# Kernel tuning notes

Hardware: AMD Instinct MI355X
Metric: run time of the kernel (lower is better)

## Reference

```python
import jax, jax.numpy as jnp
import numpy as np

N0, N1, N2 = 331776, 36864, 4096   # src nodes block0, mid nodes, final items
E0, E1, EP = 294912, 32768, 4096   # edges block0, block1, pos/neg edges
F_RAW, D, H = 128, 256, 512        # raw feat dim, hidden_dims_sum, 2*hidden
N_NODES = 1000000                  # global graph node count (scorer bias)


def setup_inputs() -> dict:
    key = jax.random.key(0)
    ks = jax.random.split(key, 24)
    ri = lambda k, n, hi: jax.random.randint(k, (n,), 0, hi, dtype=jnp.int64 if False else jnp.int32).astype(jnp.int32)
    s = 0.05
    return {
        "feat0": jax.random.normal(ks[0], (N0, F_RAW), jnp.float32),
        "feat_dst": jax.random.normal(ks[1], (N2, F_RAW), jnp.float32),
        "weights0": jax.random.uniform(ks[2], (E0,), jnp.float32),
        "weights1": jax.random.uniform(ks[3], (E1,), jnp.float32),
        "W_proj": jax.random.normal(ks[4], (F_RAW, D), jnp.float32) * s,
        "b_proj": jnp.zeros((D,), jnp.float32),
        "Q1": jax.random.normal(ks[5], (D, H), jnp.float32) * s,
        "bq1": jnp.zeros((H,), jnp.float32),
        "W1": jax.random.normal(ks[6], (D + H, D), jnp.float32) * s,
        "bw1": jnp.zeros((D,), jnp.float32),
        "Q2": jax.random.normal(ks[7], (D, H), jnp.float32) * s,
        "bq2": jnp.zeros((H,), jnp.float32),
        "W2": jax.random.normal(ks[8], (D + H, D), jnp.float32) * s,
        "bw2": jnp.zeros((D,), jnp.float32),
        "bias": jnp.zeros((N_NODES,), jnp.float32),
        "block0_src": ri(ks[9], E0, N0),
        "block0_dst": ri(ks[10], E0, N1),
        "block1_src": ri(ks[11], E1, N1),
        "block1_dst": ri(ks[12], E1, N2),
        "pos_src": ri(ks[13], EP, N2),
        "pos_dst": ri(ks[14], EP, N2),
        "neg_src": ri(ks[15], EP, N2),
        "neg_dst": ri(ks[16], EP, N2),
        "nid": ri(ks[17], N2, N_NODES),
    }


def _l2norm(z):
    n = jnp.linalg.norm(z, axis=1, keepdims=True)
    return z / jnp.where(n == 0, 1.0, n)


def _sage_conv(h_src, h_dst, src, dst, w, Q, bq, W, bw, n_dst):
    # WeightedSAGEConv (dropout omitted: eval-mode deterministic reference)
    n = jax.nn.relu(h_src @ Q + bq)                                   # [N_src, H]
    m = jax.ops.segment_sum(n[src] * w[:, None], dst, num_segments=n_dst)
    ws = jnp.clip(jax.ops.segment_sum(w, dst, num_segments=n_dst), 1.0, None)
    z = jax.nn.relu(jnp.concatenate([m / ws[:, None], h_dst], axis=1) @ W + bw)
    return _l2norm(z)


def _score(h, src, dst, nid, bias):
    # ItemToItemScorer: u_dot_v + src/dst node bias
    return jnp.sum(h[src] * h[dst], axis=1) + bias[nid[src]] + bias[nid[dst]]


def reference(feat0, feat_dst, weights0, weights1, W_proj, b_proj, Q1, bq1, W1, bw1,
              Q2, bq2, W2, bw2, bias, block0_src, block0_dst, block1_src, block1_dst,
              pos_src, pos_dst, neg_src, neg_dst, nid):
    h = feat0 @ W_proj + b_proj                                         # LinearProjector
    h = _sage_conv(h, h[:N1], block0_src, block0_dst, weights0, Q1, bq1, W1, bw1, N1)
    h = _sage_conv(h, h[:N2], block1_src, block1_dst, weights1, Q2, bq2, W2, bw2, N2)
    h_item = (feat_dst @ W_proj + b_proj) + h                           # get_repr skip-add
    pos_score = _score(h_item, pos_src, pos_dst, nid, bias)
    neg_score = _score(h_item, neg_src, neg_dst, nid, bias)
    return (pos_score, neg_score)
```

## Files before the change

### kernel.cpp

```cpp
#include <hip/hip_runtime.h>
#include <hip/hip_bf16.h>

typedef __hip_bfloat16 bf16;
typedef __attribute__((ext_vector_type(8))) short frag8;
typedef __attribute__((ext_vector_type(4))) float f32x4;

#define N0c 331776
#define N1c 36864
#define N2c 4096
#define E0c 294912
#define E1c 32768

__device__ __forceinline__ float bfbits2f(unsigned short b) {
    union { unsigned u; float f; } x; x.u = ((unsigned)b) << 16; return x.f;
}
__device__ __forceinline__ float bfval2f(const bf16* p) {
    return bfbits2f(*reinterpret_cast<const unsigned short*>(p));
}
__device__ __forceinline__ unsigned short f2bfbits(float f) {
    bf16 h = __float2bfloat16(f);
    return *reinterpret_cast<unsigned short*>(&h);
}
__device__ __forceinline__ void load4f(const float* p, float* o) {
    const float4 v = *reinterpret_cast<const float4*>(p);
    o[0] = v.x; o[1] = v.y; o[2] = v.z; o[3] = v.w;
}
__device__ __forceinline__ ushort4 pack4(float4 v) {
    ushort4 o; o.x = f2bfbits(v.x); o.y = f2bfbits(v.y);
    o.z = f2bfbits(v.z); o.w = f2bfbits(v.w); return o;
}
__device__ __forceinline__ void store_c(float* p, float v) { *p = v; }
__device__ __forceinline__ void store_c(bf16* p, float v)  { *p = __float2bfloat16(v); }
__device__ __forceinline__ f32x4 zero4() {
    f32x4 z; z[0] = 0.f; z[1] = 0.f; z[2] = 0.f; z[3] = 0.f; return z;
}
__device__ __forceinline__ f32x4 mfma16(frag8 a, frag8 b, f32x4 c) {
    return __builtin_amdgcn_mfma_f32_16x16x32_bf16(a, b, c, 0, 0, 0);
}

__global__ __launch_bounds__(256) void transpose_bf16(
    const float* __restrict__ src, bf16* __restrict__ dst, int K, int N)
{
    const int idx = blockIdx.x * 256 + threadIdx.x;
    if (idx >= K * N) return;
    const int k = idx / N, n = idx - k * N;
    dst[(size_t)n * K + k] = __float2bfloat16(src[idx]);
}

__global__ __launch_bounds__(256) void hist_kernel(
    const int* __restrict__ dst, const float* __restrict__ w,
    int* __restrict__ cnt, float* __restrict__ wsum, int E)
{
    const int e = blockIdx.x * 256 + threadIdx.x;
    if (e < E) {
        const int d = dst[e];
        atomicAdd(&cnt[d], 1);
        atomicAdd(&wsum[d], w[e]);
    }
}

__global__ __launch_bounds__(256) void invws_kernel(
    const float* __restrict__ wsum, float* __restrict__ invws, int n)
{
    const int i = blockIdx.x * 256 + threadIdx.x;
    if (i < n) invws[i] = 1.f / fmaxf(wsum[i], 1.f);
}

__global__ __launch_bounds__(1024) void scan_kernel(
    const int* __restrict__ cnt, int* __restrict__ base, int n)
{
    __shared__ int ps[1024];
    const int t = threadIdx.x;
    const int chunk = (n + 1023) >> 10;
    const int lo = t * chunk;
    const int hi = (lo + chunk < n) ? lo + chunk : n;
    int s = 0;
    for (int i = lo; i < hi; i += 4) {
        const int4 v = *reinterpret_cast<const int4*>(cnt + i);
        s += v.x + v.y + v.z + v.w;
    }
    ps[t] = s;
    __syncthreads();
    for (int off = 1; off < 1024; off <<= 1) {
        int v = (t >= off) ? ps[t - off] : 0;
        __syncthreads();
        ps[t] += v;
        __syncthreads();
    }
    int run = ps[t] - s;
    for (int i = lo; i < hi; ++i) { base[i] = run; run += cnt[i]; }
    if (t == 1023) base[n] = ps[1023];
}

__global__ __launch_bounds__(256) void fill_kernel(
    const int* __restrict__ dst, const int* __restrict__ base,
    int* __restrict__ cursor, int* __restrict__ perm, int E)
{
    const int e = blockIdx.x * 256 + threadIdx.x;
    if (e < E) {
        const int d = dst[e];
        const int p = base[d] + atomicAdd(&cursor[d], 1);
        perm[p] = e;
    }
}

template<typename TC>
__global__ __launch_bounds__(256) void gemm_mfma_proj(
    const float* __restrict__ A, const bf16* __restrict__ WpT,
    const float* __restrict__ bp, TC* __restrict__ C)
{
    __shared__ bf16 Xs[64 * 136];

    const int tid = threadIdx.x;
    const int lane = tid & 63, wave = tid >> 6;
    const int row0 = blockIdx.x * 64;

    {
        const int r = tid >> 2, q = tid & 3;
        const float* ar = A + (size_t)(row0 + r) * 128 + q * 32;
        bf16* xr = Xs + r * 136 + q * 32;
        #pragma unroll
        for (int i = 0; i < 8; ++i)
            *reinterpret_cast<ushort4*>(xr + i * 4) =
                pack4(*reinterpret_cast<const float4*>(ar + i * 4));
    }
    __syncthreads();

    const int lr = lane & 15;
    const int lk = (lane >> 4) * 8;
    const int lm4 = (lane >> 4) * 4;

    f32x4 acc[4][4];
    #pragma unroll
    for (int mi = 0; mi < 4; ++mi)
        #pragma unroll
        for (int ni = 0; ni < 4; ++ni) acc[mi][ni] = zero4();

    #pragma unroll
    for (int kk = 0; kk < 4; ++kk) {
        frag8 a[4], b[4];
        #pragma unroll
        for (int mi = 0; mi < 4; ++mi)
            a[mi] = *reinterpret_cast<const frag8*>(&Xs[(mi * 16 + lr) * 136 + kk * 32 + lk]);
        #pragma unroll
        for (int ni = 0; ni < 4; ++ni)
            b[ni] = *reinterpret_cast<const frag8*>(
                WpT + (size_t)(wave * 64 + ni * 16 + lr) * 128 + kk * 32 + lk);
        #pragma unroll
        for (int mi = 0; mi < 4; ++mi)
            #pragma unroll
            for (int ni = 0; ni < 4; ++ni)
                acc[mi][ni] = mfma16(a[mi], b[ni], acc[mi][ni]);
    }

    #pragma unroll
    for (int ni = 0; ni < 4; ++ni) {
        const int c = wave * 64 + ni * 16 + lr;
        const float bb = bp[c];
        #pragma unroll
        for (int mi = 0; mi < 4; ++mi)
            #pragma unroll
            for (int i = 0; i < 4; ++i)
                store_c(C + (size_t)(row0 + mi * 16 + lm4 + i) * 256 + c,
                        acc[mi][ni][i] + bb);
    }
}

__global__ __launch_bounds__(256) void edge_reduce_csr(
    const bf16* __restrict__ zn, const bf16* __restrict__ QT,
    const float* __restrict__ bq,
    const int* __restrict__ perm, const int* __restrict__ srcv,
    const int* __restrict__ dstv, const float* __restrict__ w,
    const float* __restrict__ invws, float* __restrict__ mout)
{
    __shared__ bf16 Zs[32 * 264];
    __shared__ bf16 Os[32 * 264];
    __shared__ int   srcs[32];
    __shared__ int   dsts[32];
    __shared__ float wts[32];

    const int tid = threadIdx.x;
    const int lane = tid & 63, wave = tid >> 6;
    const size_t p0 = (size_t)blockIdx.x * 32;

    if (tid < 32) {
        const int e = perm[p0 + tid];
        srcs[tid] = srcv[e];
        dsts[tid] = dstv[e];
        wts[tid]  = w[e];
    }
    __syncthreads();

    {
        const int r = tid >> 3, o = tid & 7;
        const int4* zr = reinterpret_cast<const int4*>(zn + (size_t)srcs[r] * 256) + o * 4;
        int4* zo = reinterpret_cast<int4*>(Zs + r * 264 + o * 32);
        #pragma unroll
        for (int i = 0; i < 4; ++i) zo[i] = zr[i];
    }
    __syncthreads();

    const int lr = lane & 15;
    const int lk = (lane >> 4) * 8;
    const int lm4 = (lane >> 4) * 4;

    for (int pass = 0; pass < 2; ++pass) {
        const int nc0 = wave * 128 + pass * 64;
        f32x4 acc[2][4];
        #pragma unroll
        for (int mi = 0; mi < 2; ++mi)
            #pragma unroll
            for (int ni = 0; ni < 4; ++ni) acc[mi][ni] = zero4();

        #pragma unroll
        for (int kk = 0; kk < 8; ++kk) {
            frag8 a[2], b[4];
            #pragma unroll
            for (int mi = 0; mi < 2; ++mi)
                a[mi] = *reinterpret_cast<const frag8*>(&Zs[(mi * 16 + lr) * 264 + kk * 32 + lk]);
            #pragma unroll
            for (int ni = 0; ni < 4; ++ni)
                b[ni] = *reinterpret_cast<const frag8*>(
                    QT + (size_t)(nc0 + ni * 16 + lr) * 256 + kk * 32 + lk);
            #pragma unroll
            for (int mi = 0; mi < 2; ++mi)
                #pragma unroll
                for (int ni = 0; ni < 4; ++ni)
                    acc[mi][ni] = mfma16(a[mi], b[ni], acc[mi][ni]);
        }

        #pragma unroll
        for (int ni = 0; ni < 4; ++ni) {
            const int gc = nc0 + ni * 16 + lr;
            const float bb = bq[gc];
            const int lc = wave * 64 + ni * 16 + lr;
            #pragma unroll
            for (int mi = 0; mi < 2; ++mi)
                #pragma unroll
                for (int i = 0; i < 4; ++i) {
                    const int row = mi * 16 + lm4 + i;
                    const float val = fmaxf(acc[mi][ni][i] + bb, 0.f) * wts[row];
                    Os[row * 264 + lc] = __float2bfloat16(val);
                }
        }
        __syncthreads();

        {
            const int L = tid;
            const int gc = (L >> 6) * 128 + pass * 64 + (L & 63);
            float a = 0.f;
            int cur = dsts[0];
            for (int r = 0; r < 32; ++r) {
                const int d = dsts[r];
                if (d != cur) {
                    atomicAdd(&mout[(size_t)cur * 512 + gc], a * invws[cur]);
                    a = 0.f; cur = d;
                }
                a += bfval2f(&Os[r * 264 + L]);
            }
            atomicAdd(&mout[(size_t)cur * 512 + gc], a * invws[cur]);
        }
        __syncthreads();
    }
}

template<typename TC>
__global__ __launch_bounds__(256) void gemm_mfma_concat(
    const float* __restrict__ m, const bf16* __restrict__ hdst,
    const bf16* __restrict__ WT, const float* __restrict__ bias,
    TC* __restrict__ C)
{
    __shared__ bf16 As[64 * 136];

    const int tid = threadIdx.x;
    const int lane = tid & 63, wave = tid >> 6;
    const int row0 = blockIdx.x * 64;
    const int r = tid >> 2, q = tid & 3;

    const int lr = lane & 15;
    const int lk = (lane >> 4) * 8;
    const int lm4 = (lane >> 4) * 4;

    f32x4 acc[4][4];
    #pragma unroll
    for (int mi = 0; mi < 4; ++mi)
        #pragma unroll
        for (int ni = 0; ni < 4; ++ni) acc[mi][ni] = zero4();

    #pragma unroll
    for (int ch = 0; ch < 6; ++ch) {
        bf16* xr = As + r * 136 + q * 32;
        if (ch < 4) {
            const float* sp = m + (size_t)(row0 + r) * 512 + ch * 128 + q * 32;
            #pragma unroll
            for (int i = 0; i < 8; ++i)
                *reinterpret_cast<ushort4*>(xr + i * 4) =
                    pack4(*reinterpret_cast<const float4*>(sp + i * 4));
        } else {
            const bf16* sp = hdst + (size_t)(row0 + r) * 256 + (ch - 4) * 128 + q * 32;
            #pragma unroll
            for (int i = 0; i < 8; ++i)
                *reinterpret_cast<ushort4*>(xr + i * 4) =
                    *reinterpret_cast<const ushort4*>(sp + i * 4);
        }
        __syncthreads();

        #pragma unroll
        for (int kk = 0; kk < 4; ++kk) {
            frag8 a[4], b[4];
            #pragma unroll
            for (int mi = 0; mi < 4; ++mi)
                a[mi] = *reinterpret_cast<const frag8*>(&As[(mi * 16 + lr) * 136 + kk * 32 + lk]);
            #pragma unroll
            for (int ni = 0; ni < 4; ++ni)
                b[ni] = *reinterpret_cast<const frag8*>(
                    WT + (size_t)(wave * 64 + ni * 16 + lr) * 768 + ch * 128 + kk * 32 + lk);
            #pragma unroll
            for (int mi = 0; mi < 4; ++mi)
                #pragma unroll
                for (int ni = 0; ni < 4; ++ni)
                    acc[mi][ni] = mfma16(a[mi], b[ni], acc[mi][ni]);
        }
        __syncthreads();
    }

    #pragma unroll
    for (int ni = 0; ni < 4; ++ni) {
        const int c = wave * 64 + ni * 16 + lr;
        const float bb = bias[c];
        #pragma unroll
        for (int mi = 0; mi < 4; ++mi)
            #pragma unroll
            for (int i = 0; i < 4; ++i)
                store_c(C + (size_t)(row0 + mi * 16 + lm4 + i) * 256 + c,
                        fmaxf(acc[mi][ni][i] + bb, 0.f));
    }
}

__global__ __launch_bounds__(256) void l2norm_kernel(
    const bf16* __restrict__ Z, bf16* __restrict__ out, int rows)
{
    const int wave = threadIdx.x >> 6, lane = threadIdx.x & 63;
    const int row = blockIdx.x * 4 + wave;
    if (row >= rows) return;
    const ushort4 u = *reinterpret_cast<const ushort4*>(Z + (size_t)row * 256 + lane * 4);
    float v[4] = { bfbits2f(u.x), bfbits2f(u.y), bfbits2f(u.z), bfbits2f(u.w) };
    float ss = v[0]*v[0] + v[1]*v[1] + v[2]*v[2] + v[3]*v[3];
    #pragma unroll
    for (int off = 32; off; off >>= 1) ss += __shfl_xor(ss, off, 64);
    const float scale = (ss == 0.f) ? 1.f : (1.f / sqrtf(ss));
    ushort4 o;
    o.x = f2bfbits(v[0]*scale); o.y = f2bfbits(v[1]*scale);
    o.z = f2bfbits(v[2]*scale); o.w = f2bfbits(v[3]*scale);
    *reinterpret_cast<ushort4*>(out + (size_t)row * 256 + lane * 4) = o;
}

__global__ __launch_bounds__(256) void l2norm_add_kernel(
    const float* __restrict__ Z, const float* __restrict__ P,
    float* __restrict__ out, int rows)
{
    const int wave = threadIdx.x >> 6, lane = threadIdx.x & 63;
    const int row = blockIdx.x * 4 + wave;
    if (row >= rows) return;
    float v[4];
    load4f(Z + (size_t)row * 256 + lane * 4, v);
    float ss = v[0]*v[0] + v[1]*v[1] + v[2]*v[2] + v[3]*v[3];
    #pragma unroll
    for (int off = 32; off; off >>= 1) ss += __shfl_xor(ss, off, 64);
    const float scale = (ss == 0.f) ? 1.f : (1.f / sqrtf(ss));
    float p[4];
    load4f(P + (size_t)row * 256 + lane * 4, p);
    float4 o;
    o.x = p[0] + v[0]*scale; o.y = p[1] + v[1]*scale;
    o.z = p[2] + v[2]*scale; o.w = p[3] + v[3]*scale;
    *reinterpret_cast<float4*>(out + (size_t)row * 256 + lane * 4) = o;
}

__global__ __launch_bounds__(256) void score_kernel(
    const float* __restrict__ h,
    const int* __restrict__ ps, const int* __restrict__ pdi,
    const int* __restrict__ ns, const int* __restrict__ nd,
    const int* __restrict__ nid, const float* __restrict__ bias,
    float* __restrict__ out)
{
    const int wave = threadIdx.x >> 6, lane = threadIdx.x & 63;
    const int e = blockIdx.x * 4 + wave;
    const int ei = e & 4095;
    const int s = (e < 4096) ? ps[ei] : ns[ei];
    const int d = (e < 4096) ? pdi[ei] : nd[ei];
    float a[4], b[4];
    load4f(h + (size_t)s * 256 + lane * 4, a);
    load4f(h + (size_t)d * 256 + lane * 4, b);
    float dot = a[0]*b[0] + a[1]*b[1] + a[2]*b[2] + a[3]*b[3];
    #pragma unroll
    for (int off = 32; off; off >>= 1) dot += __shfl_xor(dot, off, 64);
    if (lane == 0)
        out[e] = dot + bias[nid[s]] + bias[nid[d]];
}

extern "C" void kernel_launch(void* const* d_in, const int* in_sizes, int n_in,
                              void* d_out, int out_size, void* d_ws, size_t ws_size,
                              hipStream_t stream)
{
    const float* feat0    = (const float*)d_in[0];
    const float* feat_dst = (const float*)d_in[1];
    const float* weights0 = (const float*)d_in[2];
    const float* weights1 = (const float*)d_in[3];
    const float* W_proj   = (const float*)d_in[4];
    const float* b_proj   = (const float*)d_in[5];
    const float* Q1       = (const float*)d_in[6];
    const float* bq1      = (const float*)d_in[7];
    const float* W1       = (const float*)d_in[8];
    const float* bw1      = (const float*)d_in[9];
    const float* Q2       = (const float*)d_in[10];
    const float* bq2      = (const float*)d_in[11];
    const float* W2       = (const float*)d_in[12];
    const float* bw2      = (const float*)d_in[13];
    const float* biasN    = (const float*)d_in[14];
    const int* b0s = (const int*)d_in[15];
    const int* b0d = (const int*)d_in[16];
    const int* b1s = (const int*)d_in[17];
    const int* b1d = (const int*)d_in[18];
    const int* pos_src = (const int*)d_in[19];
    const int* pos_dst = (const int*)d_in[20];
    const int* neg_src = (const int*)d_in[21];
    const int* neg_dst = (const int*)d_in[22];
    const int* nid     = (const int*)d_in[23];

    char* ws = (char*)d_ws;
    size_t off = 0;
    auto alloc = [&](size_t bytes) -> void* {
        void* p = ws + off; off += (bytes + 255) & ~(size_t)255; return p;
    };
    bf16*  h0     = (bf16*) alloc((size_t)N0c * 256 * 2);
    float* m1     = (float*)alloc((size_t)N1c * 512 * 4);
    bf16*  z1b    = (bf16*) alloc((size_t)N1c * 256 * 2);
    bf16*  z1n    = (bf16*) alloc((size_t)N1c * 256 * 2);
    float* m2     = (float*)alloc((size_t)N2c * 512 * 4);
    float* z2     = (float*)alloc((size_t)N2c * 256 * 4);
    float* pdbuf  = (float*)alloc((size_t)N2c * 256 * 4);
    float* h_item = (float*)alloc((size_t)N2c * 256 * 4);
    bf16*  WpT    = (bf16*) alloc((size_t)256 * 128 * 2);
    bf16*  Q1T    = (bf16*) alloc((size_t)512 * 256 * 2);
    bf16*  Q2T    = (bf16*) alloc((size_t)512 * 256 * 2);
    bf16*  W1T    = (bf16*) alloc((size_t)256 * 768 * 2);
    bf16*  W2T    = (bf16*) alloc((size_t)256 * 768 * 2);
    int*   cnt    = (int*)  alloc((size_t)(N1c + 1) * 4);
    int*   base   = (int*)  alloc((size_t)(N1c + 1) * 4);
    int*   cursor = (int*)  alloc((size_t)N1c * 4);
    float* wsumf  = (float*)alloc((size_t)N1c * 4);
    float* invws  = (float*)alloc((size_t)N1c * 4);
    int*   perm   = (int*)  alloc((size_t)E0c * 4);

    transpose_bf16<<<(128*256 + 255)/256, 256, 0, stream>>>(W_proj, WpT, 128, 256);
    transpose_bf16<<<(256*512 + 255)/256, 256, 0, stream>>>(Q1, Q1T, 256, 512);
    transpose_bf16<<<(256*512 + 255)/256, 256, 0, stream>>>(Q2, Q2T, 256, 512);
    transpose_bf16<<<(768*256 + 255)/256, 256, 0, stream>>>(W1, W1T, 768, 256);
    transpose_bf16<<<(768*256 + 255)/256, 256, 0, stream>>>(W2, W2T, 768, 256);

    gemm_mfma_proj<bf16><<<N0c/64, 256, 0, stream>>>(feat0, WpT, b_proj, h0);

    hipMemsetAsync(cnt,    0, (size_t)N1c * 4, stream);
    hipMemsetAsync(cursor, 0, (size_t)N1c * 4, stream);
    hipMemsetAsync(wsumf,  0, (size_t)N1c * 4, stream);
    hist_kernel<<<E0c/256, 256, 0, stream>>>(b0d, weights0, cnt, wsumf, E0c);
    scan_kernel<<<1, 1024, 0, stream>>>(cnt, base, N1c);
    fill_kernel<<<E0c/256, 256, 0, stream>>>(b0d, base, cursor, perm, E0c);
    invws_kernel<<<(N1c + 255)/256, 256, 0, stream>>>(wsumf, invws, N1c);

    hipMemsetAsync(m1, 0, (size_t)N1c * 512 * 4, stream);
    edge_reduce_csr<<<E0c/32, 256, 0, stream>>>(
        h0, Q1T, bq1, perm, b0s, b0d, weights0, invws, m1);

    gemm_mfma_concat<bf16><<<N1c/64, 256, 0, stream>>>(m1, h0, W1T, bw1, z1b);
    l2norm_kernel<<<N1c/4, 256, 0, stream>>>(z1b, z1n, N1c);

    hipMemsetAsync(cnt,    0, (size_t)N2c * 4, stream);
    hipMemsetAsync(cursor, 0, (size_t)N2c * 4, stream);
    hipMemsetAsync(wsumf,  0, (size_t)N2c * 4, stream);
    hist_kernel<<<E1c/256, 256, 0, stream>>>(b1d, weights1, cnt, wsumf, E1c);
    scan_kernel<<<1, 1024, 0, stream>>>(cnt, base, N2c);
    fill_kernel<<<E1c/256, 256, 0, stream>>>(b1d, base, cursor, perm, E1c);
    invws_kernel<<<(N2c + 255)/256, 256, 0, stream>>>(wsumf, invws, N2c);

    hipMemsetAsync(m2, 0, (size_t)N2c * 512 * 4, stream);
    edge_reduce_csr<<<E1c/32, 256, 0, stream>>>(
        z1n, Q2T, bq2, perm, b1s, b1d, weights1, invws, m2);

    gemm_mfma_concat<float><<<N2c/64, 256, 0, stream>>>(m2, z1n, W2T, bw2, z2);
    gemm_mfma_proj<float><<<N2c/64, 256, 0, stream>>>(feat_dst, WpT, b_proj, pdbuf);
    l2norm_add_kernel<<<N2c/4, 256, 0, stream>>>(z2, pdbuf, h_item, N2c);

    score_kernel<<<2048, 256, 0, stream>>>(
        h_item, pos_src, pos_dst, neg_src, neg_dst, nid, biasN, (float*)d_out);
}
```

Measured before the change: 729.8 us.

## Process multiple edge tiles per block with register-prefetched gathers

The edge_reduce_csr kernel now handles four 32-edge tiles per block instead of one. While the current tile runs its MFMA and atomic reduction, the block prefetches the next tile's source-row gather into registers and the tile-after-next's edge indices, using double-buffered shared index arrays. This is meant to hide gather latency and amortize block setup, at the cost of more registers, four times fewer blocks, and extra synchronization. Runs of the same destination that cross a tile boundary still issue separate atomics.

```diff
diff --git a/kernel.cpp b/kernel.cpp
--- a/kernel.cpp
+++ b/kernel.cpp
@@ -10,6 +10,7 @@
 #define N2c 4096
 #define E0c 294912
 #define E1c 32768
+#define TILES 4
 
 __device__ __forceinline__ float bfbits2f(unsigned short b) {
     union { unsigned u; float f; } x; x.u = ((unsigned)b) << 16; return x.f;
@@ -175,28 +176,36 @@
 {
     __shared__ bf16 Zs[32 * 264];
     __shared__ bf16 Os[32 * 264];
-    __shared__ int   srcs[32];
-    __shared__ int   dsts[32];
-    __shared__ float wts[32];
+    __shared__ int   s_src[2][32];
+    __shared__ int   s_dst[2][32];
+    __shared__ float s_w[2][32];
 
     const int tid = threadIdx.x;
     const int lane = tid & 63, wave = tid >> 6;
-    const size_t p0 = (size_t)blockIdx.x * 32;
+    const size_t tile0 = (size_t)blockIdx.x * TILES;
 
     if (tid < 32) {
-        const int e = perm[p0 + tid];
-        srcs[tid] = srcv[e];
-        dsts[tid] = dstv[e];
-        wts[tid]  = w[e];
+        const int e = perm[tile0 * 32 + tid];
+        s_src[0][tid] = srcv[e];
+        s_dst[0][tid] = dstv[e];
+        s_w[0][tid]   = w[e];
     }
     __syncthreads();
 
+    const int gr = tid >> 3, go = tid & 7;
+    int4 g0, g1, g2, g3;
     {
-        const int r = tid >> 3, o = tid & 7;
-        const int4* zr = reinterpret_cast<const int4*>(zn + (size_t)srcs[r] * 256) + o * 4;
-        int4* zo = reinterpret_cast<int4*>(Zs + r * 264 + o * 32);
-        #pragma unroll
-        for (int i = 0; i < 4; ++i) zo[i] = zr[i];
+        const int4* zr = reinterpret_cast<const int4*>(zn + (size_t)s_src[0][gr] * 256) + go * 4;
+        g0 = zr[0]; g1 = zr[1]; g2 = zr[2]; g3 = zr[3];
+    }
+    int m_s = 0, m_d = 0; float m_w = 0.f;
+    if (TILES > 1 && tid < 32) {
+        const int e = perm[(tile0 + 1) * 32 + tid];
+        m_s = srcv[e]; m_d = dstv[e]; m_w = w[e];
+    }
+    {
+        int4* zo = reinterpret_cast<int4*>(Zs + gr * 264 + go * 32);
+        zo[0] = g0; zo[1] = g1; zo[2] = g2; zo[3] = g3;
     }
     __syncthreads();
 
@@ -204,63 +213,88 @@
     const int lk = (lane >> 4) * 8;
     const int lm4 = (lane >> 4) * 4;
 
-    for (int pass = 0; pass < 2; ++pass) {
-        const int nc0 = wave * 128 + pass * 64;
-        f32x4 acc[2][4];
-        #pragma unroll
-        for (int mi = 0; mi < 2; ++mi)
-            #pragma unroll
-            for (int ni = 0; ni < 4; ++ni) acc[mi][ni] = zero4();
-
-        #pragma unroll
-        for (int kk = 0; kk < 8; ++kk) {
-            frag8 a[2], b[4];
-            #pragma unroll
-            for (int mi = 0; mi < 2; ++mi)
-                a[mi] = *reinterpret_cast<const frag8*>(&Zs[(mi * 16 + lr) * 264 + kk * 32 + lk]);
-            #pragma unroll
-            for (int ni = 0; ni < 4; ++ni)
-                b[ni] = *reinterpret_cast<const frag8*>(
-                    QT + (size_t)(nc0 + ni * 16 + lr) * 256 + kk * 32 + lk);
+    for (int t = 0; t < TILES; ++t) {
+        const int cb = t & 1, nb = cb ^ 1;
+
+        if (t + 1 < TILES && tid < 32) {
+            s_src[nb][tid] = m_s; s_dst[nb][tid] = m_d; s_w[nb][tid] = m_w;
+        }
+        __syncthreads();
+
+        if (t + 1 < TILES) {
+            const int4* zr = reinterpret_cast<const int4*>(
+                zn + (size_t)s_src[nb][gr] * 256) + go * 4;
+            g0 = zr[0]; g1 = zr[1]; g2 = zr[2]; g3 = zr[3];
+        }
+        if (t + 2 < TILES && tid < 32) {
+            const int e = perm[(tile0 + t + 2) * 32 + tid];
+            m_s = srcv[e]; m_d = dstv[e]; m_w = w[e];
+        }
+
+        for (int pass = 0; pass < 2; ++pass) {
+            const int nc0 = wave * 128 + pass * 64;
+            f32x4 acc[2][4];
             #pragma unroll
             for (int mi = 0; mi < 2; ++mi)
                 #pragma unroll
+                for (int ni = 0; ni < 4; ++ni) acc[mi][ni] = zero4();
+
+            #pragma unroll
+            for (int kk = 0; kk < 8; ++kk) {
+                frag8 a[2], b[4];
+                #pragma unroll
+                for (int mi = 0; mi < 2; ++mi)
+                    a[mi] = *reinterpret_cast<const frag8*>(
+                        &Zs[(mi * 16 + lr) * 264 + kk * 32 + lk]);
+                #pragma unroll
                 for (int ni = 0; ni < 4; ++ni)
-                    acc[mi][ni] = mfma16(a[mi], b[ni], acc[mi][ni]);
+                    b[ni] = *reinterpret_cast<const frag8*>(
+                        QT + (size_t)(nc0 + ni * 16 + lr) * 256 + kk * 32 + lk);
+                #pragma unroll
+                for (int mi = 0; mi < 2; ++mi)
+                    #pragma unroll
+                    for (int ni = 0; ni < 4; ++ni)
+                        acc[mi][ni] = mfma16(a[mi], b[ni], acc[mi][ni]);
+            }
+
+            #pragma unroll
+            for (int ni = 0; ni < 4; ++ni) {
+                const int gc = nc0 + ni * 16 + lr;
+                const float bb = bq[gc];
+                const int lc = wave * 64 + ni * 16 + lr;
+                #pragma unroll
+                for (int mi = 0; mi < 2; ++mi)
+                    #pragma unroll
+                    for (int i = 0; i < 4; ++i) {
+                        const int row = mi * 16 + lm4 + i;
+                        const float val = fmaxf(acc[mi][ni][i] + bb, 0.f) * s_w[cb][row];
+                        Os[row * 264 + lc] = __float2bfloat16(val);
+                    }
+            }
+            __syncthreads();
+
+            if (pass == 1 && t + 1 < TILES) {
+                int4* zo = reinterpret_cast<int4*>(Zs + gr * 264 + go * 32);
+                zo[0] = g0; zo[1] = g1; zo[2] = g2; zo[3] = g3;
+            }
+
+            {
+                const int L = tid;
+                const int gc = (L >> 6) * 128 + pass * 64 + (L & 63);
+                float a = 0.f;
+                int cur = s_dst[cb][0];
+                for (int r = 0; r < 32; ++r) {
+                    const int d = s_dst[cb][r];
+                    if (d != cur) {
+                        atomicAdd(&mout[(size_t)cur * 512 + gc], a * invws[cur]);
+                        a = 0.f; cur = d;
+                    }
+                    a += bfval2f(&Os[r * 264 + L]);
+                }
+                atomicAdd(&mout[(size_t)cur * 512 + gc], a * invws[cur]);
+            }
+            __syncthreads();
         }
-
-        #pragma unroll
-        for (int ni = 0; ni < 4; ++ni) {
-            const int gc = nc0 + ni * 16 + lr;
-            const float bb = bq[gc];
-            const int lc = wave * 64 + ni * 16 + lr;
-            #pragma unroll
-            for (int mi = 0; mi < 2; ++mi)
-                #pragma unroll
-                for (int i = 0; i < 4; ++i) {
-                    const int row = mi * 16 + lm4 + i;
-                    const float val = fmaxf(acc[mi][ni][i] + bb, 0.f) * wts[row];
-                    Os[row * 264 + lc] = __float2bfloat16(val);
-                }
-        }
-        __syncthreads();
-
-        {
-            const int L = tid;
-            const int gc = (L >> 6) * 128 + pass * 64 + (L & 63);
-            float a = 0.f;
-            int cur = dsts[0];
-            for (int r = 0; r < 32; ++r) {
-                const int d = dsts[r];
-                if (d != cur) {
-                    atomicAdd(&mout[(size_t)cur * 512 + gc], a * invws[cur]);
-                    a = 0.f; cur = d;
-                }
-                a += bfval2f(&Os[r * 264 + L]);
-            }
-            atomicAdd(&mout[(size_t)cur * 512 + gc], a * invws[cur]);
-        }
-        __syncthreads();
     }
 }
 
@@ -469,7 +503,7 @@
     invws_kernel<<<(N1c + 255)/256, 256, 0, stream>>>(wsumf, invws, N1c);
 
     hipMemsetAsync(m1, 0, (size_t)N1c * 512 * 4, stream);
-    edge_reduce_csr<<<E0c/32, 256, 0, stream>>>(
+    edge_reduce_csr<<<E0c/(32*TILES), 256, 0, stream>>>(
         h0, Q1T, bq1, perm, b0s, b0d, weights0, invws, m1);
 
     gemm_mfma_concat<bf16><<<N1c/64, 256, 0, stream>>>(m1, h0, W1T, bw1, z1b);
@@ -484,7 +518,7 @@
     invws_kernel<<<(N2c + 255)/256, 256, 0, stream>>>(wsumf, invws, N2c);
 
     hipMemsetAsync(m2, 0, (size_t)N2c * 512 * 4, stream);
-    edge_reduce_csr<<<E1c/32, 256, 0, stream>>>(
+    edge_reduce_csr<<<E1c/(32*TILES), 256, 0, stream>>>(
         z1n, Q2T, bq2, perm, b1s, b1d, weights1, invws, m2);
 
     gemm_mfma_concat<float><<<N2c/64, 256, 0, stream>>>(m2, z1n, W2T, bw2, z2);
```

Result: slower. 803.3 us (+10.1%).

## Make edge reduce wave-independent with per-wave 16-edge tiles

Applied to the files above, without the earlier changes.

Restructures the fused edge GEMM+scatter kernel so each of the four waves owns 16 sorted edges and computes all 512 output columns itself, replacing block-wide __syncthreads with wave barriers. Each block now handles 64 edges instead of 32. This removes inter-wave synchronisation stalls, but each wave re-reads the full QT weight matrix for only 16 rows, so global weight traffic per edge doubles. Segment runs are also split at 16-edge boundaries, which can produce more atomics.

```diff
diff --git a/kernel.cpp b/kernel.cpp
--- a/kernel.cpp
+++ b/kernel.cpp
@@ -166,101 +166,100 @@
     }
 }
 
-__global__ __launch_bounds__(256) void edge_reduce_csr(
+__global__ __launch_bounds__(256) void edge_reduce_wave(
     const bf16* __restrict__ zn, const bf16* __restrict__ QT,
     const float* __restrict__ bq,
     const int* __restrict__ perm, const int* __restrict__ srcv,
     const int* __restrict__ dstv, const float* __restrict__ w,
     const float* __restrict__ invws, float* __restrict__ mout)
 {
-    __shared__ bf16 Zs[32 * 264];
-    __shared__ bf16 Os[32 * 264];
-    __shared__ int   srcs[32];
-    __shared__ int   dsts[32];
-    __shared__ float wts[32];
+    __shared__ bf16 Zs[4 * 16 * 264];
+    __shared__ bf16 Os[4 * 16 * 136];
+    __shared__ int   sS[64];
+    __shared__ int   sD[64];
+    __shared__ float sW[64];
 
     const int tid = threadIdx.x;
     const int lane = tid & 63, wave = tid >> 6;
-    const size_t p0 = (size_t)blockIdx.x * 32;
-
-    if (tid < 32) {
-        const int e = perm[p0 + tid];
-        srcs[tid] = srcv[e];
-        dsts[tid] = dstv[e];
-        wts[tid]  = w[e];
-    }
-    __syncthreads();
+    const size_t p0 = (size_t)blockIdx.x * 64 + wave * 16;
+
+    bf16*  zw = Zs + wave * (16 * 264);
+    bf16*  ow = Os + wave * (16 * 136);
+    int*   ss = sS + wave * 16;
+    int*   sd = sD + wave * 16;
+    float* sw = sW + wave * 16;
+
+    if (lane < 16) {
+        const int e = perm[p0 + lane];
+        ss[lane] = srcv[e];
+        sd[lane] = dstv[e];
+        sw[lane] = w[e];
+    }
+    __builtin_amdgcn_wave_barrier();
 
     {
-        const int r = tid >> 3, o = tid & 7;
-        const int4* zr = reinterpret_cast<const int4*>(zn + (size_t)srcs[r] * 256) + o * 4;
-        int4* zo = reinterpret_cast<int4*>(Zs + r * 264 + o * 32);
+        const int r = lane >> 2, q = lane & 3;
+        const int4* zr = reinterpret_cast<const int4*>(zn + (size_t)ss[r] * 256 + q * 64);
+        int4* zo = reinterpret_cast<int4*>(zw + r * 264 + q * 64);
         #pragma unroll
         for (int i = 0; i < 4; ++i) zo[i] = zr[i];
-    }
-    __syncthreads();
+        #pragma unroll
+        for (int i = 4; i < 8; ++i) zo[i] = zr[i];
+    }
+    __builtin_amdgcn_wave_barrier();
 
     const int lr = lane & 15;
     const int lk = (lane >> 4) * 8;
     const int lm4 = (lane >> 4) * 4;
 
-    for (int pass = 0; pass < 2; ++pass) {
-        const int nc0 = wave * 128 + pass * 64;
-        f32x4 acc[2][4];
-        #pragma unroll
-        for (int mi = 0; mi < 2; ++mi)
-            #pragma unroll
-            for (int ni = 0; ni < 4; ++ni) acc[mi][ni] = zero4();
+    for (int cp = 0; cp < 4; ++cp) {
+        const int nc0 = cp * 128;
+        f32x4 acc[8];
+        #pragma unroll
+        for (int ni = 0; ni < 8; ++ni) acc[ni] = zero4();
 
         #pragma unroll
         for (int kk = 0; kk < 8; ++kk) {
-            frag8 a[2], b[4];
-            #pragma unroll
-            for (int mi = 0; mi < 2; ++mi)
-                a[mi] = *reinterpret_cast<const frag8*>(&Zs[(mi * 16 + lr) * 264 + kk * 32 + lk]);
-            #pragma unroll
-            for (int ni = 0; ni < 4; ++ni)
-                b[ni] = *reinterpret_cast<const frag8*>(
+            const frag8 a = *reinterpret_cast<const frag8*>(&zw[lr * 264 + kk * 32 + lk]);
+            #pragma unroll
+            for (int ni = 0; ni < 8; ++ni) {
+                const frag8 b = *reinterpret_cast<const frag8*>(
                     QT + (size_t)(nc0 + ni * 16 + lr) * 256 + kk * 32 + lk);
-            #pragma unroll
-            for (int mi = 0; mi < 2; ++mi)
-                #pragma unroll
-                for (int ni = 0; ni < 4; ++ni)
-                    acc[mi][ni] = mfma16(a[mi], b[ni], acc[mi][ni]);
+                acc[ni] = mfma16(a, b, acc[ni]);
+            }
         }
 
         #pragma unroll
-        for (int ni = 0; ni < 4; ++ni) {
+        for (int ni = 0; ni < 8; ++ni) {
             const int gc = nc0 + ni * 16 + lr;
             const float bb = bq[gc];
-            const int lc = wave * 64 + ni * 16 + lr;
-            #pragma unroll
-            for (int mi = 0; mi < 2; ++mi)
-                #pragma unroll
-                for (int i = 0; i < 4; ++i) {
-                    const int row = mi * 16 + lm4 + i;
-                    const float val = fmaxf(acc[mi][ni][i] + bb, 0.f) * wts[row];
-                    Os[row * 264 + lc] = __float2bfloat16(val);
-                }
+            const int lc = ni * 16 + lr;
+            #pragma unroll
+            for (int i = 0; i < 4; ++i) {
+                const int row = lm4 + i;
+                const float val = fmaxf(acc[ni][i] + bb, 0.f) * sw[row];
+                ow[row * 136 + lc] = __float2bfloat16(val);
+            }
         }
-        __syncthreads();
-
-        {
-            const int L = tid;
-            const int gc = (L >> 6) * 128 + pass * 64 + (L & 63);
+        __builtin_amdgcn_wave_barrier();
+
+        #pragma unroll
+        for (int cidx = 0; cidx < 2; ++cidx) {
+            const int lc = lane * 2 + cidx;
+            const int gc = nc0 + lc;
             float a = 0.f;
-            int cur = dsts[0];
-            for (int r = 0; r < 32; ++r) {
-                const int d = dsts[r];
+            int cur = sd[0];
+            for (int r = 0; r < 16; ++r) {
+                const int d = sd[r];
                 if (d != cur) {
                     atomicAdd(&mout[(size_t)cur * 512 + gc], a * invws[cur]);
                     a = 0.f; cur = d;
                 }
-                a += bfval2f(&Os[r * 264 + L]);
+                a += bfval2f(&ow[r * 136 + lc]);
             }
             atomicAdd(&mout[(size_t)cur * 512 + gc], a * invws[cur]);
         }
-        __syncthreads();
+        __builtin_amdgcn_wave_barrier();
     }
 }
 
@@ -469,7 +468,7 @@
     invws_kernel<<<(N1c + 255)/256, 256, 0, stream>>>(wsumf, invws, N1c);
 
     hipMemsetAsync(m1, 0, (size_t)N1c * 512 * 4, stream);
-    edge_reduce_csr<<<E0c/32, 256, 0, stream>>>(
+    edge_reduce_wave<<<E0c/64, 256, 0, stream>>>(
         h0, Q1T, bq1, perm, b0s, b0d, weights0, invws, m1);
 
     gemm_mfma_concat<bf16><<<N1c/64, 256, 0, stream>>>(m1, h0, W1T, bw1, z1b);
@@ -484,7 +483,7 @@
     invws_kernel<<<(N2c + 255)/256, 256, 0, stream>>>(wsumf, invws, N2c);
 
     hipMemsetAsync(m2, 0, (size_t)N2c * 512 * 4, stream);
-    edge_reduce_csr<<<E1c/32, 256, 0, stream>>>(
+    edge_reduce_wave<<<E1c/64, 256, 0, stream>>>(
         z1n, Q2T, bq2, perm, b1s, b1d, weights1, invws, m2);
 
     gemm_mfma_concat<float><<<N2c/64, 256, 0, stream>>>(m2, z1n, W2T, bw2, z2);
```

Measured after the change: 994.5 us. 1.36x slower.
